# Optimization experiments

Hardware: AMD Instinct MI355X
Metric: run time of the kernel (lower is better)

Reference implementation:

```python
import jax, jax.numpy as jnp
import numpy as np

B, S, D = 1, 2048, 4096
H, KVH, DH = 32, 8, 128          # nheads, kv heads, head dim (GQA expansion = 4)
HID = 11008                       # 256 * ceil(4096 * (8/3) / 256)
EPS = 1e-5
ROPE_BASE = 10000.0


def setup_inputs() -> dict:
    key = jax.random.key(0)
    ks = jax.random.split(key, 10)
    std = 0.02
    w = lambda k, shape: jax.random.normal(k, shape, dtype=jnp.float32) * std
    return {
        "x": jax.random.normal(ks[0], (B, S, D), dtype=jnp.float32),
        "position_ids": jnp.broadcast_to(jnp.arange(S, dtype=jnp.int32), (B, S)),
        "ln_w": jnp.ones((D,), dtype=jnp.float32),
        "ffln_w": jnp.ones((D,), dtype=jnp.float32),
        "wq": w(ks[1], (D, H * DH)),
        "wk": w(ks[2], (D, KVH * DH)),
        "wv": w(ks[3], (D, KVH * DH)),
        "wo": w(ks[4], (H * DH, D)),
        "wg": w(ks[5], (D, HID)),
        "w1": w(ks[6], (D, HID)),
        "w2": w(ks[7], (HID, D)),
    }


def rmsnorm(x, w, eps=EPS):
    # LayerNormParameterized(use_mean=False, use_high_precision_pow=True)
    xf = x.astype(jnp.float32)
    var = jnp.mean(xf * xf, axis=-1, keepdims=True)
    return (xf * jax.lax.rsqrt(var + eps)).astype(x.dtype) * w


def rope(x, pos):
    # interleaved (complex-pair) rotary embedding; x: [B,S,h,DH], pos: [B,S]
    dh = x.shape[-1]
    inv_freq = 1.0 / (ROPE_BASE ** (jnp.arange(0, dh, 2, dtype=jnp.float32) / dh))
    ang = pos.astype(jnp.float32)[:, :, None, None] * inv_freq  # [B,S,1,dh/2]
    cos, sin = jnp.cos(ang), jnp.sin(ang)
    x1, x2 = x[..., 0::2], x[..., 1::2]
    return jnp.stack([x1 * cos - x2 * sin, x1 * sin + x2 * cos], axis=-1).reshape(x.shape)


def block(x, position_ids, ln_w, ffln_w, wq, wk, wv, wo, wg, w1, w2):
    # --- attention sublayer ---
    a = rmsnorm(x, ln_w)
    q = (a @ wq).reshape(B, S, H, DH)
    k = (a @ wk).reshape(B, S, KVH, DH)
    v = (a @ wv).reshape(B, S, KVH, DH)
    q = rope(q, position_ids)
    k = rope(k, position_ids)
    # GQA expansion: kv head g serves query heads [g*exp, (g+1)*exp)
    exp = H // KVH
    k_e = jnp.repeat(k, exp, axis=2)  # [B,S,H,DH]
    v_e = jnp.repeat(v, exp, axis=2)
    scores = jnp.einsum("bqhd,bkhd->bhqk", q, k_e) / np.sqrt(DH).astype(np.float32)
    causal = jnp.tril(jnp.ones((S, S), dtype=bool))
    scores = jnp.where(causal, scores, jnp.finfo(scores.dtype).min)
    p = jax.nn.softmax(scores, axis=-1)
    attn = jnp.einsum("bhqk,bkhd->bqhd", p, v_e).reshape(B, S, H * DH)
    x = x + attn @ wo
    # --- SwiGLU FFN sublayer ---
    b = rmsnorm(x, ffln_w)
    ff = (jax.nn.silu(b @ wg) * (b @ w1)) @ w2
    return x + ff


def reference(x, position_ids, ln_w, ffln_w, wq, wk, wv, wo, wg, w1, w2):
    return block(x, position_ids, ln_w, ffln_w, wq, wk, wv, wo, wg, w1, w2)
```

## Files before the change

kernel.cpp:

```cpp
#include <hip/hip_runtime.h>
#include <hip/hip_bf16.h>

typedef __bf16 bf16_t;
typedef __bf16 bf16x4 __attribute__((ext_vector_type(4)));
typedef __bf16 bf16x8 __attribute__((ext_vector_type(8)));
typedef float f32x4 __attribute__((ext_vector_type(4)));

#define S_ 2048
#define D_ 4096
#define H_ 32
#define KVH_ 8
#define DH_ 128
#define HID_ 11008
#define QKV_N 6144
#define GU_N 22016

__device__ __forceinline__ void gl16(const bf16_t* g, bf16_t* l) {
  __builtin_amdgcn_global_load_lds(
      (const __attribute__((address_space(1))) unsigned int*)g,
      (__attribute__((address_space(3))) unsigned int*)l, 16, 0, 0);
}

#define VMW(N)                                          \
  asm volatile("s_waitcnt vmcnt(" #N ")" ::: "memory"); \
  __builtin_amdgcn_sched_barrier(0)

#define LGKM(N)                                           \
  asm volatile("s_waitcnt lgkmcnt(" #N ")" ::: "memory"); \
  __builtin_amdgcn_sched_barrier(0)

#define BAR()                          \
  asm volatile("" ::: "memory");       \
  __builtin_amdgcn_s_barrier();        \
  asm volatile("" ::: "memory")

__global__ __launch_bounds__(256) void rmsnorm_kernel(
    const float* __restrict__ x, const float* __restrict__ w,
    bf16_t* __restrict__ out) {
  int row = blockIdx.x;
  const float* xr = x + (size_t)row * D_;
  float ss = 0.f;
  #pragma unroll
  for (int it = 0; it < 4; ++it) {
    int i = threadIdx.x * 4 + it * 1024;
    float4 v = *(const float4*)(xr + i);
    ss += v.x * v.x + v.y * v.y + v.z * v.z + v.w * v.w;
  }
  #pragma unroll
  for (int off = 32; off; off >>= 1) ss += __shfl_xor(ss, off);
  __shared__ float s4[4];
  if ((threadIdx.x & 63) == 0) s4[threadIdx.x >> 6] = ss;
  __syncthreads();
  float tot = s4[0] + s4[1] + s4[2] + s4[3];
  float rinv = rsqrtf(tot / (float)D_ + 1e-5f);
  bf16_t* orow = out + (size_t)row * D_;
  #pragma unroll
  for (int it = 0; it < 4; ++it) {
    int i = threadIdx.x * 4 + it * 1024;
    float4 v = *(const float4*)(xr + i);
    orow[i + 0] = (bf16_t)(v.x * rinv * w[i + 0]);
    orow[i + 1] = (bf16_t)(v.y * rinv * w[i + 1]);
    orow[i + 2] = (bf16_t)(v.z * rinv * w[i + 2]);
    orow[i + 3] = (bf16_t)(v.w * rinv * w[i + 3]);
  }
}

__global__ __launch_bounds__(256) void combine_rms_kernel(
    const float* __restrict__ x, const float* __restrict__ p0,
    const float* __restrict__ p1, const float* __restrict__ w,
    float* __restrict__ x1, bf16_t* __restrict__ out) {
  int row = blockIdx.x;
  size_t base = (size_t)row * D_;
  float ss = 0.f;
  float4 vals[4];
  #pragma unroll
  for (int it = 0; it < 4; ++it) {
    int i = threadIdx.x * 4 + it * 1024;
    float4 a = *(const float4*)(x + base + i);
    float4 b = *(const float4*)(p0 + base + i);
    float4 c = *(const float4*)(p1 + base + i);
    float4 v;
    v.x = a.x + b.x + c.x; v.y = a.y + b.y + c.y;
    v.z = a.z + b.z + c.z; v.w = a.w + b.w + c.w;
    vals[it] = v;
    *(float4*)(x1 + base + i) = v;
    ss += v.x * v.x + v.y * v.y + v.z * v.z + v.w * v.w;
  }
  #pragma unroll
  for (int off = 32; off; off >>= 1) ss += __shfl_xor(ss, off);
  __shared__ float s4[4];
  if ((threadIdx.x & 63) == 0) s4[threadIdx.x >> 6] = ss;
  __syncthreads();
  float tot = s4[0] + s4[1] + s4[2] + s4[3];
  float rinv = rsqrtf(tot / (float)D_ + 1e-5f);
  #pragma unroll
  for (int it = 0; it < 4; ++it) {
    int i = threadIdx.x * 4 + it * 1024;
    float4 v = vals[it];
    out[base + i + 0] = (bf16_t)(v.x * rinv * w[i + 0]);
    out[base + i + 1] = (bf16_t)(v.y * rinv * w[i + 1]);
    out[base + i + 2] = (bf16_t)(v.z * rinv * w[i + 2]);
    out[base + i + 3] = (bf16_t)(v.w * rinv * w[i + 3]);
  }
}

__global__ __launch_bounds__(256) void combine_out_kernel(
    const float* __restrict__ x1, const float* __restrict__ p0,
    const float* __restrict__ p1, float* __restrict__ outp) {
  size_t i = ((size_t)blockIdx.x * 256 + threadIdx.x) * 4;
  float4 a = *(const float4*)(x1 + i);
  float4 b = *(const float4*)(p0 + i);
  float4 c = *(const float4*)(p1 + i);
  float4 v;
  v.x = a.x + b.x + c.x; v.y = a.y + b.y + c.y;
  v.z = a.z + b.z + c.z; v.w = a.w + b.w + c.w;
  *(float4*)(outp + i) = v;
}

__global__ __launch_bounds__(256) void wtrans_kernel(
    const float* __restrict__ W, bf16_t* __restrict__ WT, int K, int N) {
  __shared__ bf16_t t[32][258];
  int k0 = blockIdx.x * 32, n0 = blockIdx.y * 256;
  #pragma unroll
  for (int i = 0; i < 8; ++i) {
    int flat = i * 1024 + threadIdx.x * 4;
    int kk = flat >> 8, nn = flat & 255;
    float4 wv = *(const float4*)(W + (size_t)(k0 + kk) * N + n0 + nn);
    bf16_t* p = &t[kk][nn];
    p[0] = (bf16_t)wv.x; p[1] = (bf16_t)wv.y;
    p[2] = (bf16_t)wv.z; p[3] = (bf16_t)wv.w;
  }
  __syncthreads();
  int kc8 = (threadIdx.x & 3) * 8;
  #pragma unroll
  for (int i = 0; i < 4; ++i) {
    int nn = i * 64 + (threadIdx.x >> 2);
    bf16x8 vals;
    #pragma unroll
    for (int j = 0; j < 8; ++j) vals[j] = t[kc8 + j][nn];
    *(bf16x8*)(WT + (size_t)(n0 + nn) * K + k0 + kc8) = vals;
  }
}

__global__ __launch_bounds__(256) void vtrans_kernel(
    const bf16_t* __restrict__ qkv, bf16_t* __restrict__ vt) {
  __shared__ bf16_t t[64][72];
  int s0 = blockIdx.x * 64, d0 = blockIdx.y * 64;
  #pragma unroll
  for (int it = 0; it < 2; ++it) {
    int r = (threadIdx.x >> 3) + it * 32;
    int c = (threadIdx.x & 7) * 8;
    *(bf16x8*)&t[r][c] =
        *(const bf16x8*)(qkv + (size_t)(s0 + r) * QKV_N + 5120 + d0 + c);
  }
  __syncthreads();
  #pragma unroll
  for (int it = 0; it < 2; ++it) {
    int c = threadIdx.x & 63;
    int sb = (threadIdx.x >> 6) * 16 + it * 8;
    bf16x8 v;
    #pragma unroll
    for (int j = 0; j < 8; ++j) v[j] = t[sb + j][c];
    *(bf16x8*)(vt + (size_t)(d0 + c) * S_ + s0 + sb) = v;
  }
}

__global__ __launch_bounds__(256) void rope_table_kernel(
    const int* __restrict__ pos_ids, float* __restrict__ cos_t,
    float* __restrict__ sin_t) {
  int idx = blockIdx.x * 256 + threadIdx.x;
  int s = idx >> 6, i = idx & 63;
  float pos = (float)pos_ids[s];
  float inv_freq = exp2f(-(float)i * (13.287712379549449f / 64.0f));
  float ang = pos * inv_freq;
  cos_t[idx] = cosf(ang);
  sin_t[idx] = sinf(ang);
}

__global__ __launch_bounds__(256) void rope_kernel(
    bf16_t* __restrict__ buf, const float* __restrict__ cos_t,
    const float* __restrict__ sin_t, int nheads, int colbase, int total) {
  int idx = blockIdx.x * 256 + threadIdx.x;
  if (idx >= total) return;
  int i = idx & 63;
  int t2 = idx >> 6;
  int s = t2 / nheads, h = t2 % nheads;
  size_t base = (size_t)s * QKV_N + colbase + h * 128 + 2 * i;
  float x1 = (float)buf[base], x2 = (float)buf[base + 1];
  float c = cos_t[s * 64 + i], sn = sin_t[s * 64 + i];
  buf[base]     = (bf16_t)(x1 * c - x2 * sn);
  buf[base + 1] = (bf16_t)(x1 * sn + x2 * c);
}


#define READ_A(dst, BIx, KK)                                               \
  _Pragma("unroll") for (int m = 0; m < 4; ++m)                            \
    dst[m] = *(const bf16x8*)&lds[BIx][0][KK]                              \
        [(wr * 64 + m * 16 + fr) * 32 + rc * 8];

#define READ_B(dst, BIx, KK)                                               \
  _Pragma("unroll") for (int n = 0; n < 4; ++n)                            \
    dst[n] = *(const bf16x8*)&lds[BIx][1][KK]                              \
        [(wc * 64 + n * 16 + fr) * 32 + rc * 8];

#define MFMA16(aS, bS)                                                     \
  __builtin_amdgcn_s_setprio(1);                                           \
  _Pragma("unroll") for (int m = 0; m < 4; ++m)                            \
    _Pragma("unroll") for (int n = 0; n < 4; ++n)                          \
      acc[m][n] = __builtin_amdgcn_mfma_f32_16x16x32_bf16(                 \
          aS[m], bS[n], acc[m][n], 0, 0, 0);                               \
  __builtin_amdgcn_s_setprio(0);

template <int MODE, int SPLIT>
__global__ __launch_bounds__(1024, 4) void gemm256_kernel(
    const bf16_t* __restrict__ A, int lda, const bf16_t* __restrict__ BT,
    int ldb, void* __restrict__ Cout, int ldc, int K) {
  __shared__ __align__(16) bf16_t lds[2][2][2][256 * 32];

  const int tid = threadIdx.x;
  const int lane = tid & 63;
  const int wid = tid >> 6;
  const int wr = wid >> 2;
  const int wc = wid & 3;
  const int g = lane >> 4, fr = lane & 15;
  const int rc = (g + ((fr >> 1) & 3)) & 3;

  const int nwg = gridDim.x;
  const int orig = blockIdx.x;
  int wg = (orig & 7) * (nwg >> 3) + (orig >> 3);
  int kz = 0;
  if constexpr (SPLIT) {
    const int half = nwg >> 1;
    kz = wg >= half;
    wg -= kz * half;
  }
  const int bx = wg & 7;
  const int by = wg >> 3;
  const size_t row0 = (size_t)bx * 256, col0 = (size_t)by * 256;

  const int srow = tid >> 2;
  const int schunk = ((tid & 3) - ((tid >> 3) & 3)) & 3;

  const size_t lda2 = (size_t)lda * 2, ldb2 = (size_t)ldb * 2;
  const size_t kzoff = (size_t)kz * K * 2;
  const char* aB =
      (const char*)A + (row0 + srow) * lda2 + schunk * 16 + kzoff;
  const char* bB =
      (const char*)BT + (col0 + srow) * ldb2 + schunk * 16 + kzoff;

  auto stage = [&](int bi, int ab, int kk, int kt) {
    const char* base = ab ? bB : aB;
    gl16((const bf16_t*)(base + (size_t)kt * 128 + kk * 64),
         &lds[bi][ab][kk][tid * 8]);
  };

  f32x4 acc[4][4] = {};
  bf16x8 aF[4], bF[4];
  const int NT = K / 64;

  stage(0, 0, 0, 0); stage(0, 1, 0, 0);
  stage(0, 0, 1, 0); stage(0, 1, 1, 0);
  VMW(0);
  BAR();

  for (int T = 0; T < NT; ++T) {
    const int BI = T & 1;
    const int Tp1 = T + 1 < NT;
    if (Tp1) {
      stage(BI ^ 1, 0, 0, T + 1); stage(BI ^ 1, 1, 0, T + 1);
      stage(BI ^ 1, 0, 1, T + 1); stage(BI ^ 1, 1, 1, T + 1);
    }
    READ_A(aF, BI, 0); READ_B(bF, BI, 0);
    LGKM(0);
    MFMA16(aF, bF);
    READ_A(aF, BI, 1); READ_B(bF, BI, 1);
    LGKM(0);
    MFMA16(aF, bF);
    VMW(0);
    BAR();
  }

  float* fOut = (float*)Cout + (size_t)kz * 2048 * ldc;
  #pragma unroll
  for (int m = 0; m < 4; ++m)
    #pragma unroll
    for (int n = 0; n < 4; ++n)
      #pragma unroll
      for (int r = 0; r < 4; ++r) {
        size_t row = row0 + wr * 64 + m * 16 + g * 4 + r;
        size_t col = col0 + wc * 64 + n * 16 + fr;
        float val = acc[m][n][r];
        if constexpr (MODE == 0) {
          ((bf16_t*)Cout)[row * ldc + col] = (bf16_t)val;
        } else {
          fOut[row * ldc + col] = val;
        }
      }
}

__global__ __launch_bounds__(256, 2) void attn_kernel(
    const bf16_t* __restrict__ qkv, const bf16_t* __restrict__ vt,
    bf16_t* __restrict__ o) {
  int h = blockIdx.y;
  int qb = (S_ / 64 - 1) - blockIdx.x;
  int kvh = h >> 2;
  int tid = threadIdx.x;
  int wid = tid >> 6, lane = tid & 63;
  int g = lane >> 4, fr = lane & 15;

  __shared__ __align__(16) bf16_t kfl[2][8192];
  __shared__ __align__(16) bf16_t vfl[2][8192];
  __shared__ __align__(16) bf16_t p_lds[4][16][72];

  const int fr_s = (tid >> 2) & 15, g_s = tid & 3;
  const int kcw = (tid >> 6) & 3;
  const int kc2w = (tid >> 6) & 1;
  const int nhi = tid >> 7;
  const bf16_t* kSrc = qkv + (size_t)fr_s * QKV_N + 4096 + kvh * 128 +
                       (kcw * 4 + g_s) * 8;
  const bf16_t* vSrc = vt + ((size_t)kvh * 128 + nhi * 16 + fr_s) * S_ +
                       (kc2w * 4 + g_s) * 8;

  auto stage = [&](int bi, int t) {
    size_t kv0 = (size_t)t * 64;
    #pragma unroll
    for (int i = 0; i < 4; ++i)
      gl16(kSrc + (kv0 + i * 16) * QKV_N, &kfl[bi][(i * 256 + tid) * 8]);
    #pragma unroll
    for (int i = 0; i < 4; ++i)
      gl16(vSrc + (size_t)i * 32 * S_ + kv0, &vfl[bi][(i * 256 + tid) * 8]);
  };

  int q0w = qb * 64 + wid * 16;
  bf16x8 q_frag[4];
  const bf16_t* qptr = qkv + (size_t)(q0w + fr) * QKV_N + h * 128;
  #pragma unroll
  for (int kc = 0; kc < 4; ++kc)
    q_frag[kc] = *(const bf16x8*)(qptr + kc * 32 + g * 8);
  VMW(0);

  stage(0, 0);

  f32x4 o_frag[8] = {};
  float m_run[4], l_run[4];
  #pragma unroll
  for (int r = 0; r < 4; ++r) { m_run[r] = -1e30f; l_run[r] = 0.f; }

  const float sc = 0.08838834764831845f * 1.4426950408889634f;

  for (int t = 0; t <= qb; ++t) {
    int cur = t & 1;
    int kv0 = t * 64;
    if (t < qb) {
      stage(cur ^ 1, t + 1);
      VMW(8);
    } else {
      VMW(0);
    }
    BAR();

    f32x4 sfr[4];
    #pragma unroll
    for (int nf = 0; nf < 4; ++nf) {
      f32x4 acc = {};
      #pragma unroll
      for (int kc = 0; kc < 4; ++kc) {
        bf16x8 kf =
            *(const bf16x8*)&kfl[cur][(nf * 256 + kc * 64 + fr * 4 + g) * 8];
        acc = __builtin_amdgcn_mfma_f32_16x16x32_bf16(q_frag[kc], kf, acc, 0, 0, 0);
      }
      sfr[nf] = acc;
    }

    bool diag = (t == qb);
    float mtile[4];
    #pragma unroll
    for (int r = 0; r < 4; ++r) mtile[r] = -1e30f;
    #pragma unroll
    for (int nf = 0; nf < 4; ++nf)
      #pragma unroll
      for (int r = 0; r < 4; ++r) {
        if (diag) {
          int kvg = kv0 + nf * 16 + fr;
          int qg = q0w + 4 * g + r;
          if (kvg > qg) sfr[nf][r] = -1e30f;
        }
        mtile[r] = fmaxf(mtile[r], sfr[nf][r]);
      }
    #pragma unroll
    for (int r = 0; r < 4; ++r) {
      float mv = mtile[r];
      mv = fmaxf(mv, __shfl_xor(mv, 1));
      mv = fmaxf(mv, __shfl_xor(mv, 2));
      mv = fmaxf(mv, __shfl_xor(mv, 4));
      mv = fmaxf(mv, __shfl_xor(mv, 8));
      mtile[r] = mv;
    }
    float alpha[4];
    #pragma unroll
    for (int r = 0; r < 4; ++r) {
      float m_new = fmaxf(m_run[r], mtile[r]);
      alpha[r] = exp2f((m_run[r] - m_new) * sc);
      m_run[r] = m_new;
    }
    float lsum[4] = {0.f, 0.f, 0.f, 0.f};
    #pragma unroll
    for (int nf = 0; nf < 4; ++nf)
      #pragma unroll
      for (int r = 0; r < 4; ++r) {
        float p = exp2f((sfr[nf][r] - m_run[r]) * sc);
        sfr[nf][r] = p;
        lsum[r] += p;
      }
    #pragma unroll
    for (int r = 0; r < 4; ++r) {
      float lv = lsum[r];
      lv += __shfl_xor(lv, 1);
      lv += __shfl_xor(lv, 2);
      lv += __shfl_xor(lv, 4);
      lv += __shfl_xor(lv, 8);
      l_run[r] = l_run[r] * alpha[r] + lv;
    }
    #pragma unroll
    for (int nfo = 0; nfo < 8; ++nfo)
      #pragma unroll
      for (int r = 0; r < 4; ++r) o_frag[nfo][r] *= alpha[r];

    #pragma unroll
    for (int nf = 0; nf < 4; ++nf)
      #pragma unroll
      for (int r = 0; r < 4; ++r)
        p_lds[wid][4 * g + r][nf * 16 + fr] = (bf16_t)sfr[nf][r];

    #pragma unroll
    for (int kc2 = 0; kc2 < 2; ++kc2) {
      bf16x8 pf = *(const bf16x8*)&p_lds[wid][fr][kc2 * 32 + g * 8];
      #pragma unroll
      for (int nfo = 0; nfo < 8; ++nfo) {
        bf16x8 vf =
            *(const bf16x8*)&vfl[cur][(nfo * 128 + kc2 * 64 + fr * 4 + g) * 8];
        o_frag[nfo] = __builtin_amdgcn_mfma_f32_16x16x32_bf16(pf, vf, o_frag[nfo], 0, 0, 0);
      }
    }
    BAR();
  }

  #pragma unroll
  for (int nfo = 0; nfo < 8; ++nfo)
    #pragma unroll
    for (int r = 0; r < 4; ++r) {
      int qg = q0w + 4 * g + r;
      float val = o_frag[nfo][r] / l_run[r];
      o[(size_t)qg * (H_ * DH_) + h * DH_ + nfo * 16 + fr] = (bf16_t)val;
    }
}

__global__ __launch_bounds__(256) void silu_mul_kernel(bf16_t* __restrict__ gu) {
  size_t idx = (size_t)blockIdx.x * 256 + threadIdx.x;
  int r = (int)(idx / (HID_ / 8));
  int c8 = (int)(idx % (HID_ / 8));
  bf16_t* p = gu + (size_t)r * GU_N + c8 * 8;
  bf16x8 g8 = *(const bf16x8*)p;
  bf16x8 u8 = *(const bf16x8*)(p + HID_);
  bf16x8 h8;
  #pragma unroll
  for (int j = 0; j < 8; ++j) {
    float gv = (float)g8[j];
    float uv = (float)u8[j];
    h8[j] = (bf16_t)(gv / (1.f + __expf(-gv)) * uv);
  }
  *(bf16x8*)p = h8;
}

extern "C" void kernel_launch(void* const* d_in, const int* in_sizes, int n_in,
                              void* d_out, int out_size, void* d_ws,
                              size_t ws_size, hipStream_t stream) {
  const float* x = (const float*)d_in[0];
  const int* pos = (const int*)d_in[1];
  const float* ln_w = (const float*)d_in[2];
  const float* ffln_w = (const float*)d_in[3];
  const float* wq = (const float*)d_in[4];
  const float* wk = (const float*)d_in[5];
  const float* wv = (const float*)d_in[6];
  const float* wo = (const float*)d_in[7];
  const float* wg = (const float*)d_in[8];
  const float* w1 = (const float*)d_in[9];
  const float* w2 = (const float*)d_in[10];

  char* ws = (char*)d_ws;
  size_t off = 0;
  auto alloc = [&](size_t bytes) {
    size_t o = off;
    off = (off + bytes + 255) & ~(size_t)255;
    return o;
  };
  bf16_t* Wbuf = (bf16_t*)(ws + alloc((size_t)GU_N * D_ * 2));
  bf16_t* nbuf = (bf16_t*)(ws + alloc((size_t)S_ * D_ * 2));
  bf16_t* qkv  = (bf16_t*)(ws + alloc((size_t)S_ * QKV_N * 2));
  float*  x1   = (float*)(ws + alloc((size_t)S_ * D_ * 4));
  bf16_t* gu   = (bf16_t*)(ws + alloc((size_t)S_ * GU_N * 2));
  bf16_t* vtb  = (bf16_t*)(ws + alloc((size_t)KVH_ * DH_ * S_ * 2));
  float*  cos_t = (float*)(ws + alloc((size_t)S_ * 64 * 4));
  float*  sin_t = (float*)(ws + alloc((size_t)S_ * 64 * 4));
  float* part = (float*)((char*)Wbuf + ((size_t)96 << 20));

  rmsnorm_kernel<<<S_, 256, 0, stream>>>(x, ln_w, nbuf);
  wtrans_kernel<<<dim3(D_ / 32, D_ / 256), 256, 0, stream>>>(wq, Wbuf, D_, D_);
  wtrans_kernel<<<dim3(D_ / 32, 1024 / 256), 256, 0, stream>>>(
      wk, Wbuf + (size_t)4096 * D_, D_, 1024);
  wtrans_kernel<<<dim3(D_ / 32, 1024 / 256), 256, 0, stream>>>(
      wv, Wbuf + (size_t)5120 * D_, D_, 1024);
  rope_table_kernel<<<(S_ * 64) / 256, 256, 0, stream>>>(pos, cos_t, sin_t);
  gemm256_kernel<0, 0><<<dim3((S_ / 256) * (QKV_N / 256)), 1024, 0, stream>>>(
      nbuf, D_, Wbuf, D_, qkv, QKV_N, D_);
  rope_kernel<<<(S_ * H_ * 64) / 256, 256, 0, stream>>>(
      qkv, cos_t, sin_t, H_, 0, S_ * H_ * 64);
  rope_kernel<<<(S_ * KVH_ * 64) / 256, 256, 0, stream>>>(
      qkv, cos_t, sin_t, KVH_, 4096, S_ * KVH_ * 64);
  vtrans_kernel<<<dim3(S_ / 64, (KVH_ * DH_) / 64), 256, 0, stream>>>(qkv, vtb);
  attn_kernel<<<dim3(S_ / 64, H_), 256, 0, stream>>>(qkv, vtb, nbuf);
  wtrans_kernel<<<dim3(D_ / 32, D_ / 256), 256, 0, stream>>>(wo, Wbuf, D_, D_);
  gemm256_kernel<2, 1><<<dim3((S_ / 256) * (D_ / 256) * 2), 1024, 0, stream>>>(
      nbuf, D_, Wbuf, D_, part, D_, 2048);
  combine_rms_kernel<<<S_, 256, 0, stream>>>(
      x, part, part + (size_t)S_ * D_, ffln_w, x1, nbuf);
  wtrans_kernel<<<dim3(D_ / 32, HID_ / 256), 256, 0, stream>>>(wg, Wbuf, D_, HID_);
  wtrans_kernel<<<dim3(D_ / 32, HID_ / 256), 256, 0, stream>>>(
      w1, Wbuf + (size_t)HID_ * D_, D_, HID_);
  gemm256_kernel<0, 0><<<dim3((S_ / 256) * (GU_N / 256)), 1024, 0, stream>>>(
      nbuf, D_, Wbuf, D_, gu, GU_N, D_);
  silu_mul_kernel<<<(S_ * HID_ / 8) / 256, 256, 0, stream>>>(gu);
  wtrans_kernel<<<dim3(HID_ / 32, D_ / 256), 256, 0, stream>>>(w2, Wbuf, HID_, D_);
  gemm256_kernel<2, 1><<<dim3((S_ / 256) * (D_ / 256) * 2), 1024, 0, stream>>>(
      gu, GU_N, Wbuf, HID_, part, D_, 5504);
  combine_out_kernel<<<(S_ * D_ / 4) / 256, 256, 0, stream>>>(
      x1, part, part + (size_t)S_ * D_, (float*)d_out);
}
```

Measured before the change: 1.194 ms.

## Interleave LDS fragment reads with MFMA groups in the 256-tile GEMM loop

Restructures the GEMM inner loop so LDS fragment reads for the next k-slice and the next tile are issued in small groups between MFMA batches. Partial lgkmcnt waits replace the full drains before each 16-MFMA block. The first k-slice of the next tile is prefetched right after the barrier. The goal is to hide LDS read latency behind matrix-core work, at the cost of more hand-tuned scheduling barriers and tighter register reuse.

```diff
diff --git a/kernel.cpp b/kernel.cpp
--- a/kernel.cpp
+++ b/kernel.cpp
@@ -28,6 +28,8 @@
 #define LGKM(N)                                           \
   asm volatile("s_waitcnt lgkmcnt(" #N ")" ::: "memory"); \
   __builtin_amdgcn_sched_barrier(0)
+
+#define SB() __builtin_amdgcn_sched_barrier(0)
 
 #define BAR()                          \
   asm volatile("" ::: "memory");       \
@@ -193,23 +195,36 @@
 }
 
 
-#define READ_A(dst, BIx, KK)                                               \
-  _Pragma("unroll") for (int m = 0; m < 4; ++m)                            \
-    dst[m] = *(const bf16x8*)&lds[BIx][0][KK]                              \
-        [(wr * 64 + m * 16 + fr) * 32 + rc * 8];
-
-#define READ_B(dst, BIx, KK)                                               \
-  _Pragma("unroll") for (int n = 0; n < 4; ++n)                            \
-    dst[n] = *(const bf16x8*)&lds[BIx][1][KK]                              \
-        [(wc * 64 + n * 16 + fr) * 32 + rc * 8];
-
-#define MFMA16(aS, bS)                                                     \
+#define READ_An(m, BIx, KK)                                                \
+  aF[m] = *(const bf16x8*)&lds[BIx][0][KK]                                 \
+      [(wr * 64 + (m) * 16 + fr) * 32 + rc * 8];
+
+#define READ_Bn(n, BIx, KK)                                                \
+  bF[n] = *(const bf16x8*)&lds[BIx][1][KK]                                 \
+      [(wc * 64 + (n) * 16 + fr) * 32 + rc * 8];
+
+#define GRP_N(n)                                                           \
   __builtin_amdgcn_s_setprio(1);                                           \
   _Pragma("unroll") for (int m = 0; m < 4; ++m)                            \
-    _Pragma("unroll") for (int n = 0; n < 4; ++n)                          \
-      acc[m][n] = __builtin_amdgcn_mfma_f32_16x16x32_bf16(                 \
-          aS[m], bS[n], acc[m][n], 0, 0, 0);                               \
-  __builtin_amdgcn_s_setprio(0);
+    acc[m][n] = __builtin_amdgcn_mfma_f32_16x16x32_bf16(                   \
+        aF[m], bF[n], acc[m][n], 0, 0, 0);                                 \
+  __builtin_amdgcn_s_setprio(0);                                           \
+  SB();
+
+#define GRP_M(m)                                                           \
+  __builtin_amdgcn_s_setprio(1);                                           \
+  _Pragma("unroll") for (int n = 0; n < 4; ++n)                            \
+    acc[m][n] = __builtin_amdgcn_mfma_f32_16x16x32_bf16(                   \
+        aF[m], bF[n], acc[m][n], 0, 0, 0);                                 \
+  __builtin_amdgcn_s_setprio(0);                                           \
+  SB();
+
+#define ISSUE_KK0(BIx)                                                     \
+  READ_Bn(0, BIx, 0);                                                      \
+  READ_An(0, BIx, 0); READ_An(1, BIx, 0);                                  \
+  READ_An(2, BIx, 0); READ_An(3, BIx, 0);                                  \
+  READ_Bn(1, BIx, 0); READ_Bn(2, BIx, 0); READ_Bn(3, BIx, 0);              \
+  SB();
 
 template <int MODE, int SPLIT>
 __global__ __launch_bounds__(1024, 4) void gemm256_kernel(
@@ -262,6 +277,7 @@
   stage(0, 0, 1, 0); stage(0, 1, 1, 0);
   VMW(0);
   BAR();
+  ISSUE_KK0(0);
 
   for (int T = 0; T < NT; ++T) {
     const int BI = T & 1;
@@ -269,15 +285,23 @@
     if (Tp1) {
       stage(BI ^ 1, 0, 0, T + 1); stage(BI ^ 1, 1, 0, T + 1);
       stage(BI ^ 1, 0, 1, T + 1); stage(BI ^ 1, 1, 1, T + 1);
-    }
-    READ_A(aF, BI, 0); READ_B(bF, BI, 0);
-    LGKM(0);
-    MFMA16(aF, bF);
-    READ_A(aF, BI, 1); READ_B(bF, BI, 1);
-    LGKM(0);
-    MFMA16(aF, bF);
+      SB();
+    }
+    LGKM(3); GRP_N(0); READ_Bn(0, BI, 1); SB();
+    LGKM(3); GRP_N(1); READ_Bn(1, BI, 1); SB();
+    LGKM(3); GRP_N(2); READ_Bn(2, BI, 1); SB();
+    LGKM(3); GRP_N(3);
+    READ_Bn(3, BI, 1);
+    READ_An(0, BI, 1); READ_An(1, BI, 1);
+    READ_An(2, BI, 1); READ_An(3, BI, 1);
+    SB();
+    LGKM(3); GRP_M(0);
+    LGKM(2); GRP_M(1);
+    LGKM(1); GRP_M(2);
+    LGKM(0); GRP_M(3);
     VMW(0);
     BAR();
+    if (Tp1) { ISSUE_KK0(BI ^ 1); }
   }
 
   float* fOut = (float*)Cout + (size_t)kz * 2048 * ldc;
```

Result: no change. 1.186 ms (-0.7%).

## Fuse RoPE into QKV GEMM epilogue and SwiGLU into gate/up GEMM epilogue

Applied to the files above, without the earlier changes.

RoPE is now applied in the QKV GEMM epilogue: each lane swaps its value with its pair partner via a lane shuffle and multiplies by the cos/sin table, which replaces two standalone rope kernels. The gate and up weights are interleaved row by row in the transposed weight buffer, so each gate/up pair lands in adjacent columns. The GEMM epilogue then computes silu(g)*u and writes a half-width h buffer, which removes the silu_mul kernel and the full gu round trip through memory. Costs are extra shuffles and cos/sin loads in the epilogue, and the write-back becomes sparser, since only even lanes store in the fused SwiGLU path.

```diff
diff --git a/kernel.cpp b/kernel.cpp
--- a/kernel.cpp
+++ b/kernel.cpp
@@ -28,6 +28,8 @@
 #define LGKM(N)                                           \
   asm volatile("s_waitcnt lgkmcnt(" #N ")" ::: "memory"); \
   __builtin_amdgcn_sched_barrier(0)
+
+#define SB() __builtin_amdgcn_sched_barrier(0)
 
 #define BAR()                          \
   asm volatile("" ::: "memory");       \
@@ -118,7 +120,8 @@
 }
 
 __global__ __launch_bounds__(256) void wtrans_kernel(
-    const float* __restrict__ W, bf16_t* __restrict__ WT, int K, int N) {
+    const float* __restrict__ W, bf16_t* __restrict__ WT, int K, int N,
+    int rstride, int roff) {
   __shared__ bf16_t t[32][258];
   int k0 = blockIdx.x * 32, n0 = blockIdx.y * 256;
   #pragma unroll
@@ -138,7 +141,7 @@
     bf16x8 vals;
     #pragma unroll
     for (int j = 0; j < 8; ++j) vals[j] = t[kc8 + j][nn];
-    *(bf16x8*)(WT + (size_t)(n0 + nn) * K + k0 + kc8) = vals;
+    *(bf16x8*)(WT + ((size_t)(n0 + nn) * rstride + roff) * K + k0 + kc8) = vals;
   }
 }
 
@@ -177,21 +180,6 @@
   sin_t[idx] = sinf(ang);
 }
 
-__global__ __launch_bounds__(256) void rope_kernel(
-    bf16_t* __restrict__ buf, const float* __restrict__ cos_t,
-    const float* __restrict__ sin_t, int nheads, int colbase, int total) {
-  int idx = blockIdx.x * 256 + threadIdx.x;
-  if (idx >= total) return;
-  int i = idx & 63;
-  int t2 = idx >> 6;
-  int s = t2 / nheads, h = t2 % nheads;
-  size_t base = (size_t)s * QKV_N + colbase + h * 128 + 2 * i;
-  float x1 = (float)buf[base], x2 = (float)buf[base + 1];
-  float c = cos_t[s * 64 + i], sn = sin_t[s * 64 + i];
-  buf[base]     = (bf16_t)(x1 * c - x2 * sn);
-  buf[base + 1] = (bf16_t)(x1 * sn + x2 * c);
-}
-
 
 #define READ_A(dst, BIx, KK)                                               \
   _Pragma("unroll") for (int m = 0; m < 4; ++m)                            \
@@ -214,7 +202,8 @@
 template <int MODE, int SPLIT>
 __global__ __launch_bounds__(1024, 4) void gemm256_kernel(
     const bf16_t* __restrict__ A, int lda, const bf16_t* __restrict__ BT,
-    int ldb, void* __restrict__ Cout, int ldc, int K) {
+    int ldb, void* __restrict__ Cout, int ldc, int K,
+    const float* __restrict__ cosT, const float* __restrict__ sinT) {
   __shared__ __align__(16) bf16_t lds[2][2][2][256 * 32];
 
   const int tid = threadIdx.x;
@@ -292,8 +281,23 @@
         float val = acc[m][n][r];
         if constexpr (MODE == 0) {
           ((bf16_t*)Cout)[row * ldc + col] = (bf16_t)val;
+        } else if constexpr (MODE == 2) {
+          fOut[row * ldc + col] = val;
+        } else if constexpr (MODE == 3) {
+          float p = __shfl_xor(val, 1);
+          if ((int)col < 5120) {
+            int i = ((int)col & 127) >> 1;
+            float c = cosT[row * 64 + i], s = sinT[row * 64 + i];
+            val = (fr & 1) ? (p * s + val * c) : (val * c - p * s);
+          }
+          ((bf16_t*)Cout)[row * ldc + col] = (bf16_t)val;
         } else {
-          fOut[row * ldc + col] = val;
+          float p = __shfl_xor(val, 1);
+          if (!(fr & 1)) {
+            float gv = val;
+            float hv = gv / (1.f + __expf(-gv)) * p;
+            ((bf16_t*)Cout)[row * ldc + (col >> 1)] = (bf16_t)hv;
+          }
         }
       }
 }
@@ -453,23 +457,6 @@
       float val = o_frag[nfo][r] / l_run[r];
       o[(size_t)qg * (H_ * DH_) + h * DH_ + nfo * 16 + fr] = (bf16_t)val;
     }
-}
-
-__global__ __launch_bounds__(256) void silu_mul_kernel(bf16_t* __restrict__ gu) {
-  size_t idx = (size_t)blockIdx.x * 256 + threadIdx.x;
-  int r = (int)(idx / (HID_ / 8));
-  int c8 = (int)(idx % (HID_ / 8));
-  bf16_t* p = gu + (size_t)r * GU_N + c8 * 8;
-  bf16x8 g8 = *(const bf16x8*)p;
-  bf16x8 u8 = *(const bf16x8*)(p + HID_);
-  bf16x8 h8;
-  #pragma unroll
-  for (int j = 0; j < 8; ++j) {
-    float gv = (float)g8[j];
-    float uv = (float)u8[j];
-    h8[j] = (bf16_t)(gv / (1.f + __expf(-gv)) * uv);
-  }
-  *(bf16x8*)p = h8;
 }
 
 extern "C" void kernel_launch(void* const* d_in, const int* in_sizes, int n_in,
@@ -498,41 +485,40 @@
   bf16_t* nbuf = (bf16_t*)(ws + alloc((size_t)S_ * D_ * 2));
   bf16_t* qkv  = (bf16_t*)(ws + alloc((size_t)S_ * QKV_N * 2));
   float*  x1   = (float*)(ws + alloc((size_t)S_ * D_ * 4));
-  bf16_t* gu   = (bf16_t*)(ws + alloc((size_t)S_ * GU_N * 2));
+  bf16_t* h    = (bf16_t*)(ws + alloc((size_t)S_ * HID_ * 2));
   bf16_t* vtb  = (bf16_t*)(ws + alloc((size_t)KVH_ * DH_ * S_ * 2));
   float*  cos_t = (float*)(ws + alloc((size_t)S_ * 64 * 4));
   float*  sin_t = (float*)(ws + alloc((size_t)S_ * 64 * 4));
   float* part = (float*)((char*)Wbuf + ((size_t)96 << 20));
 
   rmsnorm_kernel<<<S_, 256, 0, stream>>>(x, ln_w, nbuf);
-  wtrans_kernel<<<dim3(D_ / 32, D_ / 256), 256, 0, stream>>>(wq, Wbuf, D_, D_);
+  wtrans_kernel<<<dim3(D_ / 32, D_ / 256), 256, 0, stream>>>(
+      wq, Wbuf, D_, D_, 1, 0);
   wtrans_kernel<<<dim3(D_ / 32, 1024 / 256), 256, 0, stream>>>(
-      wk, Wbuf + (size_t)4096 * D_, D_, 1024);
+      wk, Wbuf + (size_t)4096 * D_, D_, 1024, 1, 0);
   wtrans_kernel<<<dim3(D_ / 32, 1024 / 256), 256, 0, stream>>>(
-      wv, Wbuf + (size_t)5120 * D_, D_, 1024);
+      wv, Wbuf + (size_t)5120 * D_, D_, 1024, 1, 0);
   rope_table_kernel<<<(S_ * 64) / 256, 256, 0, stream>>>(pos, cos_t, sin_t);
-  gemm256_kernel<0, 0><<<dim3((S_ / 256) * (QKV_N / 256)), 1024, 0, stream>>>(
-      nbuf, D_, Wbuf, D_, qkv, QKV_N, D_);
-  rope_kernel<<<(S_ * H_ * 64) / 256, 256, 0, stream>>>(
-      qkv, cos_t, sin_t, H_, 0, S_ * H_ * 64);
-  rope_kernel<<<(S_ * KVH_ * 64) / 256, 256, 0, stream>>>(
-      qkv, cos_t, sin_t, KVH_, 4096, S_ * KVH_ * 64);
+  gemm256_kernel<3, 0><<<dim3((S_ / 256) * (QKV_N / 256)), 1024, 0, stream>>>(
+      nbuf, D_, Wbuf, D_, qkv, QKV_N, D_, cos_t, sin_t);
   vtrans_kernel<<<dim3(S_ / 64, (KVH_ * DH_) / 64), 256, 0, stream>>>(qkv, vtb);
   attn_kernel<<<dim3(S_ / 64, H_), 256, 0, stream>>>(qkv, vtb, nbuf);
-  wtrans_kernel<<<dim3(D_ / 32, D_ / 256), 256, 0, stream>>>(wo, Wbuf, D_, D_);
+  wtrans_kernel<<<dim3(D_ / 32, D_ / 256), 256, 0, stream>>>(
+      wo, Wbuf, D_, D_, 1, 0);
   gemm256_kernel<2, 1><<<dim3((S_ / 256) * (D_ / 256) * 2), 1024, 0, stream>>>(
-      nbuf, D_, Wbuf, D_, part, D_, 2048);
+      nbuf, D_, Wbuf, D_, part, D_, 2048, nullptr, nullptr);
   combine_rms_kernel<<<S_, 256, 0, stream>>>(
       x, part, part + (size_t)S_ * D_, ffln_w, x1, nbuf);
-  wtrans_kernel<<<dim3(D_ / 32, HID_ / 256), 256, 0, stream>>>(wg, Wbuf, D_, HID_);
   wtrans_kernel<<<dim3(D_ / 32, HID_ / 256), 256, 0, stream>>>(
-      w1, Wbuf + (size_t)HID_ * D_, D_, HID_);
-  gemm256_kernel<0, 0><<<dim3((S_ / 256) * (GU_N / 256)), 1024, 0, stream>>>(
-      nbuf, D_, Wbuf, D_, gu, GU_N, D_);
-  silu_mul_kernel<<<(S_ * HID_ / 8) / 256, 256, 0, stream>>>(gu);
-  wtrans_kernel<<<dim3(HID_ / 32, D_ / 256), 256, 0, stream>>>(w2, Wbuf, HID_, D_);
+      wg, Wbuf, D_, HID_, 2, 0);
+  wtrans_kernel<<<dim3(D_ / 32, HID_ / 256), 256, 0, stream>>>(
+      w1, Wbuf, D_, HID_, 2, 1);
+  gemm256_kernel<4, 0><<<dim3((S_ / 256) * (GU_N / 256)), 1024, 0, stream>>>(
+      nbuf, D_, Wbuf, D_, h, HID_, D_, nullptr, nullptr);
+  wtrans_kernel<<<dim3(HID_ / 32, D_ / 256), 256, 0, stream>>>(
+      w2, Wbuf, HID_, D_, 1, 0);
   gemm256_kernel<2, 1><<<dim3((S_ / 256) * (D_ / 256) * 2), 1024, 0, stream>>>(
-      gu, GU_N, Wbuf, HID_, part, D_, 5504);
+      h, HID_, Wbuf, HID_, part, D_, 5504, nullptr, nullptr);
   combine_out_kernel<<<(S_ * D_ / 4) / 256, 256, 0, stream>>>(
       x1, part, part + (size_t)S_ * D_, (float*)d_out);
 }
```

Result: no change. 1.179 ms, median of 2 (-1.3%).
